# Performance work log

Measured on AMD Instinct MI355X. Metric: run time of the kernel, lower is better.

The kernel has to match this reference:

```python
import jax, jax.numpy as jnp
import numpy as np

MAX_GRAPH_SIZE = 512
HEADS = 8
DIM_HEAD = 32

N, D = 8192, 256
G, MN = 16, 512
E = 131072


def setup_inputs() -> dict:
    key = jax.random.key(0)
    ks = jax.random.split(key, 10)
    node_feature = jax.random.normal(ks[0], (N, D), jnp.float32)
    edge_feature = jax.random.normal(ks[1], (E, D), jnp.float32) * 0.1
    edge_index = jax.random.randint(ks[2], (2, E), 0, N)
    batch = (jnp.arange(N) // (N // G)).astype(jnp.int32)  # sorted graph ids, 512 nodes/graph
    dist = jax.random.randint(ks[3], (G, MN, MN), 0, MAX_GRAPH_SIZE).astype(jnp.int32)
    centrality = jax.random.normal(ks[4], (MAX_GRAPH_SIZE, D), jnp.float32) * 0.02
    dist_bias = jax.random.normal(ks[5], (MAX_GRAPH_SIZE, HEADS), jnp.float32) * 0.02
    Wq = jax.random.normal(ks[6], (D, HEADS * DIM_HEAD), jnp.float32) * 0.05
    Wkv = jax.random.normal(ks[7], (D, 2 * HEADS * DIM_HEAD), jnp.float32) * 0.05
    Wo = jax.random.normal(ks[8], (HEADS * DIM_HEAD, D), jnp.float32) * 0.05
    bo = jax.random.normal(ks[9], (D,), jnp.float32) * 0.05
    return dict(node_feature=node_feature, edge_feature=edge_feature,
                centrality=centrality, dist_bias=dist_bias,
                Wq=Wq, Wkv=Wkv, Wo=Wo, bo=bo,
                edge_index=edge_index, batch=batch, dist=dist)


def reference(node_feature, edge_feature, centrality, dist_bias, Wq, Wkv, Wo, bo,
              edge_index, batch, dist):
    n_nodes = node_feature.shape[0]
    g, mn = dist.shape[0], dist.shape[1]
    h, dh = HEADS, DIM_HEAD
    scale = dh ** -0.5

    src = edge_index[0]
    # node degree -> centrality encoding lookup (clipped to table size)
    deg = jax.ops.segment_sum(jnp.ones((src.shape[0],), jnp.int32), src,
                              num_segments=n_nodes)
    deg = jnp.minimum(deg, MAX_GRAPH_SIZE - 1)
    # scatter-add edge features onto source nodes
    edge_out = jax.ops.segment_sum(edge_feature, src, num_segments=n_nodes)
    x = node_feature + centrality[deg] + edge_out  # [N, D]

    # dense-batch pack (to_dense_batch): position of each node within its graph
    counts = jax.ops.segment_sum(jnp.ones((n_nodes,), jnp.int32), batch, num_segments=g)
    starts = jnp.cumsum(counts) - counts  # exclusive cumsum
    pos = jnp.arange(n_nodes, dtype=jnp.int32) - starts[batch]
    dense = jnp.zeros((g, mn, x.shape[1]), x.dtype).at[batch, pos].set(x)
    mask = jnp.zeros((g, mn), bool).at[batch, pos].set(True)

    # relative-distance attention bias lookup
    dist_c = jnp.minimum(dist, MAX_GRAPH_SIZE - 1)
    sim_bias = dist_bias[dist_c]  # [G, MN, MN, H]

    # multi-head attention
    q = jnp.einsum('bnd,de->bne', dense, Wq).reshape(g, mn, h, dh)
    kv = jnp.einsum('bnd,de->bne', dense, Wkv)
    k, v = jnp.split(kv, 2, axis=-1)
    k = k.reshape(g, mn, h, dh)
    v = v.reshape(g, mn, h, dh)
    sim = jnp.einsum('bihd,bjhd->bhij', q, k) * scale
    sim = sim + jnp.transpose(sim_bias, (0, 3, 1, 2))
    sim = jnp.where(mask[:, None, None, :], sim, -jnp.inf)
    attn = jax.nn.softmax(sim, axis=-1)
    out = jnp.einsum('bhij,bjhd->bihd', attn, v).reshape(g, mn, h * dh)
    pred = jnp.einsum('bne,ed->bnd', out, Wo) + bo  # [G, MN, D]

    # ragged unpack; original loop skips the last graph (off-by-one), nodes of
    # the last graph stay zero — replicated faithfully.
    new_node_features = pred[batch, pos]
    new_node_features = jnp.where((batch < g - 1)[:, None], new_node_features, 0.0)
    return new_node_features
```

## Files before the change

kernel.cpp:

```cpp
#include <hip/hip_runtime.h>
#include <hip/hip_bf16.h>
#include <math.h>

constexpr int N_   = 8192;
constexpr int D_   = 256;
constexpr int E_   = 131072;
constexpr int G_   = 16;
constexpr int MN_  = 512;
constexpr int H_   = 8;
constexpr int MAXG_= 512;

typedef __attribute__((ext_vector_type(8))) short short8v;
typedef _Float16 half8v __attribute__((ext_vector_type(8)));
typedef __attribute__((ext_vector_type(4))) float f32x4;

__device__ inline ushort f2bf(float f) {
    unsigned u = __float_as_uint(f);
    return (ushort)((u + 0x7FFFu + ((u >> 16) & 1u)) >> 16);
}
__device__ inline float bf2f(ushort h) { return __uint_as_float((unsigned)h << 16); }
__device__ inline ushort f2h(float f) {
    _Float16 h = (_Float16)f; ushort u; __builtin_memcpy(&u, &h, 2); return u;
}
__device__ inline unsigned pack_h2(float a, float b) {
    auto h = __builtin_amdgcn_cvt_pkrtz(a, b);
    unsigned u; __builtin_memcpy(&u, &h, 4); return u;
}

__global__ void k_prep0(int* __restrict__ deg, int* __restrict__ bstart) {
    int i = blockIdx.x * 256 + threadIdx.x;
    if (i < N_) deg[i] = 0;
    if (i < G_) bstart[i] = -1;
}

__device__ void wt_dev(const float* __restrict__ W, int ncols,
                       ushort* __restrict__ wth, ushort* __restrict__ wtl,
                       int bx, int by) {
    __shared__ float tile[32][33];
    int c0 = bx * 32, k0 = by * 32;
    int t = threadIdx.x;
    int tr = t >> 5, tc = t & 31;
#pragma unroll
    for (int i = 0; i < 4; ++i)
        tile[tr * 4 + i][tc] = W[(size_t)(k0 + tr * 4 + i) * ncols + c0 + tc];
    __syncthreads();
    int cr = t >> 3, kq = (t & 7) * 4;
    ushort4 hh, ll;
    float v;
    v = tile[kq + 0][cr]; hh.x = f2bf(v); ll.x = f2bf(v - bf2f(hh.x));
    v = tile[kq + 1][cr]; hh.y = f2bf(v); ll.y = f2bf(v - bf2f(hh.y));
    v = tile[kq + 2][cr]; hh.z = f2bf(v); ll.z = f2bf(v - bf2f(hh.z));
    v = tile[kq + 3][cr]; hh.w = f2bf(v); ll.w = f2bf(v - bf2f(hh.w));
    *(ushort4*)(wth + (size_t)(c0 + cr) * 256 + k0 + kq) = hh;
    *(ushort4*)(wtl + (size_t)(c0 + cr) * 256 + k0 + kq) = ll;
}

__global__ __launch_bounds__(256) void k_prep1(
    const int* __restrict__ src, int* __restrict__ deg,
    const int* __restrict__ batch, int* __restrict__ bstart,
    const float* __restrict__ Wq, const float* __restrict__ Wkv,
    const float* __restrict__ Wo,
    ushort* __restrict__ wt_h, ushort* __restrict__ wt_l,
    ushort* __restrict__ wot_h, ushort* __restrict__ wot_l) {
    int bid = blockIdx.x;
    if (bid < 512) {
        int e = bid * 256 + threadIdx.x;
        atomicAdd(deg + src[e], 1);
    } else if (bid < 544) {
        int n = (bid - 512) * 256 + threadIdx.x;
        int g = batch[n];
        if (n == 0 || batch[n - 1] != g) bstart[g] = n;
    } else {
        int wid = bid - 544;
        if (wid < 64)        wt_dev(Wq,  256, wt_h, wt_l, wid & 7, wid >> 3);
        else if (wid < 192)  wt_dev(Wkv, 512, wt_h + 256 * 256, wt_l + 256 * 256,
                                    (wid - 64) & 15, (wid - 64) >> 4);
        else                 wt_dev(Wo,  256, wot_h, wot_l, (wid - 192) & 7, (wid - 192) >> 3);
    }
}

__global__ void k_prep2(const int* __restrict__ bstart, int* __restrict__ starts,
                        int* __restrict__ counts, const int* __restrict__ deg,
                        int* __restrict__ offs, int* __restrict__ cursor) {
    int t = threadIdx.x;
    if (t == 0) {
        int next = N_;
        for (int g = G_ - 1; g >= 0; --g) {
            int b = bstart[g];
            int s = (b >= 0) ? b : next;
            starts[g] = s;
            counts[g] = next - s;
            next = s;
        }
    }
    __shared__ int sums[256];
    int base = t * 32;
    int local[32];
    int s = 0;
#pragma unroll
    for (int k = 0; k < 32; ++k) { local[k] = deg[base + k]; s += local[k]; }
    sums[t] = s;
    __syncthreads();
    for (int off = 1; off < 256; off <<= 1) {
        int v = (t >= off) ? sums[t - off] : 0;
        __syncthreads();
        sums[t] += v;
        __syncthreads();
    }
    int acc = sums[t] - s;
#pragma unroll
    for (int k = 0; k < 32; ++k) {
        offs[base + k] = acc;
        cursor[base + k] = acc;
        acc += local[k];
    }
}

__global__ void k_fill_csr(const int* __restrict__ src, int* __restrict__ cursor,
                           int* __restrict__ eids) {
    int e = blockIdx.x * 256 + threadIdx.x;
    if (e < E_) {
        int slot = atomicAdd(cursor + src[e], 1);
        eids[slot] = e;
    }
}

__global__ void k_build_dense(const float* __restrict__ nf, const float* __restrict__ cent,
                              const float* __restrict__ ef, const int* __restrict__ deg,
                              const int* __restrict__ offs, const int* __restrict__ eids,
                              const int* __restrict__ batch, const int* __restrict__ starts,
                              ushort* __restrict__ xh, ushort* __restrict__ xl) {
    int t  = blockIdx.x * 256 + threadIdx.x;
    int n  = t >> 6;
    int c4 = (t & 63) * 4;
    if (n >= N_) return;
    int g = batch[n];
    int p = n - starts[g];
    if (p >= MN_) return;
    int row = g * MN_ + p;
    int dn = deg[n];
    int dg = min(dn, MAXG_ - 1);
    float4 a = *(const float4*)(nf   + (size_t)n  * D_ + c4);
    float4 b = *(const float4*)(cent + (size_t)dg * D_ + c4);
    float4 o;
    o.x = a.x + b.x; o.y = a.y + b.y; o.z = a.z + b.z; o.w = a.w + b.w;
    int beg = offs[n], end = beg + dn;
    int idx = beg;
    for (; idx + 4 <= end; idx += 4) {
        int e0 = eids[idx], e1 = eids[idx + 1], e2 = eids[idx + 2], e3 = eids[idx + 3];
        float4 v0 = *(const float4*)(ef + (size_t)e0 * D_ + c4);
        float4 v1 = *(const float4*)(ef + (size_t)e1 * D_ + c4);
        float4 v2 = *(const float4*)(ef + (size_t)e2 * D_ + c4);
        float4 v3 = *(const float4*)(ef + (size_t)e3 * D_ + c4);
        o.x += v0.x; o.y += v0.y; o.z += v0.z; o.w += v0.w;
        o.x += v1.x; o.y += v1.y; o.z += v1.z; o.w += v1.w;
        o.x += v2.x; o.y += v2.y; o.z += v2.z; o.w += v2.w;
        o.x += v3.x; o.y += v3.y; o.z += v3.z; o.w += v3.w;
    }
    for (; idx < end; ++idx) {
        int e = eids[idx];
        float4 v = *(const float4*)(ef + (size_t)e * D_ + c4);
        o.x += v.x; o.y += v.y; o.z += v.z; o.w += v.w;
    }
    ushort4 hh, ll;
    hh.x = f2bf(o.x); ll.x = f2bf(o.x - bf2f(hh.x));
    hh.y = f2bf(o.y); ll.y = f2bf(o.y - bf2f(hh.y));
    hh.z = f2bf(o.z); ll.z = f2bf(o.z - bf2f(hh.z));
    hh.w = f2bf(o.w); ll.w = f2bf(o.w - bf2f(hh.w));
    *(ushort4*)(xh + (size_t)row * D_ + c4) = hh;
    *(ushort4*)(xl + (size_t)row * D_ + c4) = ll;
}

__global__ __launch_bounds__(256) void k_gemm_qkv(
    const ushort* __restrict__ xh, const ushort* __restrict__ xl,
    const ushort* __restrict__ wth, const ushort* __restrict__ wtl,
    ushort* __restrict__ qh, ushort* __restrict__ qlo,
    ushort* __restrict__ kh, ushort* __restrict__ klo,
    ushort* __restrict__ vt) {
    int w = threadIdx.x >> 6, lane = threadIdx.x & 63;
    int l15 = lane & 15, quad = lane >> 4;
    int m0 = blockIdx.x * 128 + w * 32;
    int nc0 = blockIdx.y * 64;
    f32x4 acc[2][4] = {};
    const ushort* a0h = xh + (size_t)(m0 + l15) * 256 + quad * 8;
    const ushort* a0l = xl + (size_t)(m0 + l15) * 256 + quad * 8;
    for (int kc = 0; kc < 256; kc += 32) {
        short8v ah0 = *(const short8v*)(a0h + kc);
        short8v al0 = *(const short8v*)(a0l + kc);
        short8v ah1 = *(const short8v*)(a0h + 16 * 256 + kc);
        short8v al1 = *(const short8v*)(a0l + 16 * 256 + kc);
#pragma unroll
        for (int c = 0; c < 4; ++c) {
            size_t bo = (size_t)(nc0 + c * 16 + l15) * 256 + kc + quad * 8;
            short8v bh = *(const short8v*)(wth + bo);
            short8v bl = *(const short8v*)(wtl + bo);
            acc[0][c] = __builtin_amdgcn_mfma_f32_16x16x32_bf16(al0, bh, acc[0][c], 0, 0, 0);
            acc[0][c] = __builtin_amdgcn_mfma_f32_16x16x32_bf16(ah0, bl, acc[0][c], 0, 0, 0);
            acc[0][c] = __builtin_amdgcn_mfma_f32_16x16x32_bf16(ah0, bh, acc[0][c], 0, 0, 0);
            acc[1][c] = __builtin_amdgcn_mfma_f32_16x16x32_bf16(al1, bh, acc[1][c], 0, 0, 0);
            acc[1][c] = __builtin_amdgcn_mfma_f32_16x16x32_bf16(ah1, bl, acc[1][c], 0, 0, 0);
            acc[1][c] = __builtin_amdgcn_mfma_f32_16x16x32_bf16(ah1, bh, acc[1][c], 0, 0, 0);
        }
    }
    int seg = nc0 >> 8;
#pragma unroll
    for (int t = 0; t < 2; ++t) {
        int m0t = m0 + t * 16;
        int g = m0t >> 9;
        int r0 = m0t + quad * 4;
#pragma unroll
        for (int c = 0; c < 4; ++c) {
            int col = nc0 + c * 16 + l15;
            if (seg == 0) {
#pragma unroll
                for (int r = 0; r < 4; ++r) {
                    float v = acc[t][c][r];
                    ushort hh = f2bf(v);
                    qh [(size_t)(r0 + r) * 256 + col] = hh;
                    qlo[(size_t)(r0 + r) * 256 + col] = f2bf(v - bf2f(hh));
                }
            } else if (seg == 1) {
                int cc = col - 256;
#pragma unroll
                for (int r = 0; r < 4; ++r) {
                    float v = acc[t][c][r];
                    ushort hh = f2bf(v);
                    kh [(size_t)(r0 + r) * 256 + cc] = hh;
                    klo[(size_t)(r0 + r) * 256 + cc] = f2bf(v - bf2f(hh));
                }
            } else {
                int cv = col - 512;
                int h = cv >> 5, d = cv & 31;
                int j0 = (m0t & 511) + quad * 4;
                ushort4 vv;
                vv.x = f2h(acc[t][c][0]); vv.y = f2h(acc[t][c][1]);
                vv.z = f2h(acc[t][c][2]); vv.w = f2h(acc[t][c][3]);
                *(ushort4*)(vt + ((size_t)((g * 8 + h) * 32 + d)) * 512 + j0) = vv;
            }
        }
    }
}

__global__ __launch_bounds__(512) void k_attn_fused(
    const ushort* __restrict__ qh, const ushort* __restrict__ qlo,
    const ushort* __restrict__ kh, const ushort* __restrict__ klo,
    const ushort* __restrict__ vt,
    const int* __restrict__ dist, const float* __restrict__ dist_bias,
    const int* __restrict__ starts, const int* __restrict__ counts,
    const ushort* __restrict__ woth, const ushort* __restrict__ wotl,
    const float* __restrict__ bo, float* __restrict__ out)
{
    __shared__ ushort dist_lds[32][272];
    __shared__ ushort olo_lds[32][264];
    __shared__ float  biasH[8][516];

    int bid = blockIdx.x;
    int b = (bid & 7) * 32 + (bid >> 3);
    int g  = b >> 4;
    int ib = (b & 15) * 32;
    int w    = threadIdx.x >> 6;
    int lane = threadIdx.x & 63;
    int l15  = lane & 15, quad = lane >> 4;
    int h = w;
    const float scale2 = 0.17677669529663687f * 1.4426950408889634f;
    const float LOG2E  = 1.4426950408889634f;

    for (int idx = threadIdx.x; idx < 4096; idx += 512)
        biasH[idx & 7][idx >> 3] = dist_bias[idx] * LOG2E;
    {
        int r = threadIdx.x >> 4;
        int c0 = (threadIdx.x & 15) * 32;
        const int* drow = dist + ((size_t)(g * 512 + ib + r)) * 512 + c0;
#pragma unroll
        for (int u = 0; u < 32; u += 8) {
            int4 da = *(const int4*)(drow + u);
            int4 db = *(const int4*)(drow + u + 4);
            ushort4 s0, s1;
            s0.x = (ushort)min(da.x, 511); s0.y = (ushort)min(da.y, 511);
            s0.z = (ushort)min(da.z, 511); s0.w = (ushort)min(da.w, 511);
            s1.x = (ushort)min(db.x, 511); s1.y = (ushort)min(db.y, 511);
            s1.z = (ushort)min(db.z, 511); s1.w = (ushort)min(db.w, 511);
            *(ushort4*)&dist_lds[r][c0 + u]     = s0;
            *(ushort4*)&dist_lds[r][c0 + u + 4] = s1;
        }
    }
    __syncthreads();
    int cnt = counts[g];

    size_t qoff = ((size_t)(g * 512 + ib + l15)) * 256 + h * 32 + quad * 8;
    short8v qfh0 = *(const short8v*)(qh  + qoff);
    short8v qfl0 = *(const short8v*)(qlo + qoff);
    short8v qfh1 = *(const short8v*)(qh  + qoff + 16 * 256);
    short8v qfl1 = *(const short8v*)(qlo + qoff + 16 * 256);

    float m0s = -INFINITY, l0s = 0.f, m1s = -INFINITY, l1s = 0.f;
    f32x4 t0a0 = {0.f,0.f,0.f,0.f}, t0a1 = {0.f,0.f,0.f,0.f};
    f32x4 t1a0 = {0.f,0.f,0.f,0.f}, t1a1 = {0.f,0.f,0.f,0.f};

    const ushort* vbase = vt + ((size_t)((g * 8 + h) * 32)) * 512;
    size_t krowb = (size_t)(g * 512);

    auto tile_step = [&](int jb, int rowoff, bool full, short8v qfh, short8v qfl,
                         float& m, float& lsum, f32x4& a0, f32x4& a1,
                         short8v kfh0, short8v kfl0, short8v kfh1, short8v kfl1,
                         half8v v0, half8v v1) {
        float p[8];
        f32x4 c0 = {0.f,0.f,0.f,0.f};
        c0 = __builtin_amdgcn_mfma_f32_16x16x32_bf16(kfl0, qfh, c0, 0, 0, 0);
        c0 = __builtin_amdgcn_mfma_f32_16x16x32_bf16(kfh0, qfl, c0, 0, 0, 0);
        c0 = __builtin_amdgcn_mfma_f32_16x16x32_bf16(kfh0, qfh, c0, 0, 0, 0);
        f32x4 c1 = {0.f,0.f,0.f,0.f};
        c1 = __builtin_amdgcn_mfma_f32_16x16x32_bf16(kfl1, qfh, c1, 0, 0, 0);
        c1 = __builtin_amdgcn_mfma_f32_16x16x32_bf16(kfh1, qfl, c1, 0, 0, 0);
        c1 = __builtin_amdgcn_mfma_f32_16x16x32_bf16(kfh1, qfh, c1, 0, 0, 0);
        ushort4 d0 = *(const ushort4*)&dist_lds[rowoff + l15][jb + quad * 4];
        ushort4 d1 = *(const ushort4*)&dist_lds[rowoff + l15][jb + 16 + quad * 4];
        const ushort* dr0 = (const ushort*)&d0;
        const ushort* dr1 = (const ushort*)&d1;
        if (full) {
#pragma unroll
            for (int r = 0; r < 4; ++r) p[r]     = c0[r] * scale2 + biasH[h][dr0[r]];
#pragma unroll
            for (int r = 0; r < 4; ++r) p[4 + r] = c1[r] * scale2 + biasH[h][dr1[r]];
        } else {
#pragma unroll
            for (int r = 0; r < 4; ++r) {
                float s = c0[r] * scale2 + biasH[h][dr0[r]];
                p[r] = ((jb + quad * 4 + r) < cnt) ? s : -1e30f;
            }
#pragma unroll
            for (int r = 0; r < 4; ++r) {
                float s = c1[r] * scale2 + biasH[h][dr1[r]];
                p[4 + r] = ((jb + 16 + quad * 4 + r) < cnt) ? s : -1e30f;
            }
        }
        float mx = fmaxf(fmaxf(fmaxf(p[0], p[1]), fmaxf(p[2], p[3])),
                         fmaxf(fmaxf(p[4], p[5]), fmaxf(p[6], p[7])));
        mx = fmaxf(mx, __shfl_xor(mx, 16));
        mx = fmaxf(mx, __shfl_xor(mx, 32));
        float mnew = fmaxf(m, mx);
        float corr = exp2f(m - mnew);
        m = mnew;
        float m10 = m - 10.f;
        if (full) {
#pragma unroll
            for (int u = 0; u < 8; ++u) p[u] = exp2f(p[u] - m10);
        } else {
#pragma unroll
            for (int u = 0; u < 8; ++u)
                p[u] = (p[u] > -1e29f) ? exp2f(p[u] - m10) : 0.f;
        }
        float psum = ((p[0] + p[1]) + (p[2] + p[3])) + ((p[4] + p[5]) + (p[6] + p[7]));
        psum += __shfl_xor(psum, 16);
        psum += __shfl_xor(psum, 32);
        lsum = lsum * corr + psum;
#pragma unroll
        for (int r = 0; r < 4; ++r) {
            float cr = __shfl(corr, quad * 4 + r);
            a0[r] *= cr; a1[r] *= cr;
        }
        unsigned pk0A = pack_h2(p[0], p[1]), pk1A = pack_h2(p[2], p[3]);
        unsigned pk0B = pack_h2(p[4], p[5]), pk1B = pack_h2(p[6], p[7]);
        int srcA = l15 + 16 * (2 * (quad & 1));
        int srcB = srcA + 16;
        unsigned w0A = __shfl((int)pk0A, srcA), w1A = __shfl((int)pk1A, srcA);
        unsigned w2A = __shfl((int)pk0A, srcB), w3A = __shfl((int)pk1A, srcB);
        unsigned w0B = __shfl((int)pk0B, srcA), w1B = __shfl((int)pk1B, srcA);
        unsigned w2B = __shfl((int)pk0B, srcB), w3B = __shfl((int)pk1B, srcB);
        bool hiT = (quad >= 2);
        union { unsigned u[4]; half8v h; } pu;
        pu.u[0] = hiT ? w0B : w0A;
        pu.u[1] = hiT ? w1B : w1A;
        pu.u[2] = hiT ? w2B : w2A;
        pu.u[3] = hiT ? w3B : w3A;
        half8v pa = pu.h;
        a0 = __builtin_amdgcn_mfma_f32_16x16x32_f16(pa, v0, a0, 0, 0, 0);
        a1 = __builtin_amdgcn_mfma_f32_16x16x32_f16(pa, v1, a1, 0, 0, 0);
    };

    for (int jb = 0; jb < 512; jb += 32) {
        bool full = (jb + 32 <= cnt);
        size_t koff = (krowb + jb + l15) * 256 + h * 32 + quad * 8;
        short8v kfh0 = *(const short8v*)(kh  + koff);
        short8v kfl0 = *(const short8v*)(klo + koff);
        short8v kfh1 = *(const short8v*)(kh  + koff + 16 * 256);
        short8v kfl1 = *(const short8v*)(klo + koff + 16 * 256);
        half8v v0 = *(const half8v*)(vbase + (size_t)l15 * 512 + jb + quad * 8);
        half8v v1 = *(const half8v*)(vbase + (size_t)(l15 + 16) * 512 + jb + quad * 8);
        tile_step(jb, 0,  full, qfh0, qfl0, m0s, l0s, t0a0, t0a1,
                  kfh0, kfl0, kfh1, kfl1, v0, v1);
        tile_step(jb, 16, full, qfh1, qfl1, m1s, l1s, t1a0, t1a1,
                  kfh0, kfl0, kfh1, kfl1, v0, v1);
    }
    float inv0 = l0s > 0.f ? 1.f / l0s : 0.f;
    float inv1 = l1s > 0.f ? 1.f / l1s : 0.f;

    __syncthreads();
    ushort* oh_lds = &dist_lds[0][0];
    ushort* ol_lds = &olo_lds[0][0];
#pragma unroll
    for (int r = 0; r < 4; ++r) {
        float ir0 = __shfl(inv0, quad * 4 + r);
        float ir1 = __shfl(inv1, quad * 4 + r);
        int i0 = quad * 4 + r;
        int i1 = 16 + quad * 4 + r;
        float o00 = t0a0[r] * ir0, o01 = t0a1[r] * ir0;
        float o10 = t1a0[r] * ir1, o11 = t1a1[r] * ir1;
        ushort h00 = f2bf(o00), h01 = f2bf(o01), h10 = f2bf(o10), h11 = f2bf(o11);
        oh_lds[i0 * 264 + h * 32 + l15]      = h00;
        ol_lds[i0 * 264 + h * 32 + l15]      = f2bf(o00 - bf2f(h00));
        oh_lds[i0 * 264 + h * 32 + 16 + l15] = h01;
        ol_lds[i0 * 264 + h * 32 + 16 + l15] = f2bf(o01 - bf2f(h01));
        oh_lds[i1 * 264 + h * 32 + l15]      = h10;
        ol_lds[i1 * 264 + h * 32 + l15]      = f2bf(o10 - bf2f(h10));
        oh_lds[i1 * 264 + h * 32 + 16 + l15] = h11;
        ol_lds[i1 * 264 + h * 32 + 16 + l15] = f2bf(o11 - bf2f(h11));
    }
    __syncthreads();

    f32x4 pacc[2][2] = {};
    for (int kc = 0; kc < 256; kc += 32) {
        short8v ah0 = *(const short8v*)(oh_lds + l15 * 264 + kc + quad * 8);
        short8v al0 = *(const short8v*)(ol_lds + l15 * 264 + kc + quad * 8);
        short8v ah1 = *(const short8v*)(oh_lds + (l15 + 16) * 264 + kc + quad * 8);
        short8v al1 = *(const short8v*)(ol_lds + (l15 + 16) * 264 + kc + quad * 8);
#pragma unroll
        for (int cc = 0; cc < 2; ++cc) {
            int col = w * 32 + cc * 16 + l15;
            size_t bof = (size_t)col * 256 + kc + quad * 8;
            short8v bh = *(const short8v*)(woth + bof);
            short8v bl = *(const short8v*)(wotl + bof);
            pacc[0][cc] = __builtin_amdgcn_mfma_f32_16x16x32_bf16(al0, bh, pacc[0][cc], 0, 0, 0);
            pacc[0][cc] = __builtin_amdgcn_mfma_f32_16x16x32_bf16(ah0, bl, pacc[0][cc], 0, 0, 0);
            pacc[0][cc] = __builtin_amdgcn_mfma_f32_16x16x32_bf16(ah0, bh, pacc[0][cc], 0, 0, 0);
            pacc[1][cc] = __builtin_amdgcn_mfma_f32_16x16x32_bf16(al1, bh, pacc[1][cc], 0, 0, 0);
            pacc[1][cc] = __builtin_amdgcn_mfma_f32_16x16x32_bf16(ah1, bl, pacc[1][cc], 0, 0, 0);
            pacc[1][cc] = __builtin_amdgcn_mfma_f32_16x16x32_bf16(ah1, bh, pacc[1][cc], 0, 0, 0);
        }
    }
    int st = starts[g];
    bool lastg = (g == G_ - 1);
#pragma unroll
    for (int rg = 0; rg < 2; ++rg) {
#pragma unroll
        for (int cc = 0; cc < 2; ++cc) {
            int col = w * 32 + cc * 16 + l15;
            float bias = bo[col];
#pragma unroll
            for (int r = 0; r < 4; ++r) {
                int prow = ib + rg * 16 + quad * 4 + r;
                if (prow < cnt)
                    out[(size_t)(st + prow) * 256 + col] = lastg ? 0.f : (pacc[rg][cc][r] + bias);
            }
        }
    }
}

extern "C" void kernel_launch(void* const* d_in, const int* in_sizes, int n_in,
                              void* d_out, int out_size, void* d_ws, size_t ws_size,
                              hipStream_t stream) {
    const float* node_feature = (const float*)d_in[0];
    const float* edge_feature = (const float*)d_in[1];
    const float* centrality   = (const float*)d_in[2];
    const float* dist_bias    = (const float*)d_in[3];
    const float* Wq           = (const float*)d_in[4];
    const float* Wkv          = (const float*)d_in[5];
    const float* Wo           = (const float*)d_in[6];
    const float* bo           = (const float*)d_in[7];
    const int*   edge_index   = (const int*)d_in[8];
    const int*   batch        = (const int*)d_in[9];
    const int*   dist         = (const int*)d_in[10];
    float* out = (float*)d_out;

    const size_t ND = (size_t)N_ * D_;
    ushort* xh   = (ushort*)d_ws;
    ushort* xl   = xh  + ND;
    ushort* qh   = xl  + ND;
    ushort* qlo  = qh  + ND;
    ushort* kh   = qlo + ND;
    ushort* klo  = kh  + ND;
    ushort* vt   = klo + ND;
    ushort* wt_h = vt  + ND;
    ushort* wt_l = wt_h + (size_t)768 * 256;
    ushort* wot_h= wt_l + (size_t)768 * 256;
    ushort* wot_l= wot_h + (size_t)256 * 256;
    int* deg    = (int*)(wot_l + (size_t)256 * 256);
    int* bstart = deg + N_;
    int* counts = bstart + G_;
    int* starts = counts + G_;
    int* offs   = starts + G_;
    int* cursor = offs + N_;
    int* eids   = cursor + N_;

    const int* src = edge_index;

    k_prep0<<<N_ / 256, 256, 0, stream>>>(deg, bstart);
    k_prep1<<<800, 256, 0, stream>>>(src, deg, batch, bstart, Wq, Wkv, Wo,
                                     wt_h, wt_l, wot_h, wot_l);
    k_prep2<<<1, 256, 0, stream>>>(bstart, starts, counts, deg, offs, cursor);
    k_fill_csr<<<E_ / 256, 256, 0, stream>>>(src, cursor, eids);
    k_build_dense<<<(N_ * 64) / 256, 256, 0, stream>>>(node_feature, centrality, edge_feature,
                                                       deg, offs, eids, batch, starts, xh, xl);
    k_gemm_qkv<<<dim3(64, 12), 256, 0, stream>>>(xh, xl, wt_h, wt_l,
                                                 qh, qlo, kh, klo, vt);
    k_attn_fused<<<256, 512, 0, stream>>>(qh, qlo, kh, klo, vt, dist, dist_bias,
                                          starts, counts, wot_h, wot_l, bo, out);
}
```

Before: 139.6 us.

## Split fused attention into per-head split-K attention plus separate output projection GEMM

The fused attention kernel, which processed all 8 heads of a 32-row block in one 512-thread workgroup and did the output projection in LDS, is replaced. Attention now runs with one workgroup per (graph, head, 64-row block), and the key range is split between wave pairs whose softmax partial states are merged through LDS. This gives 1024 smaller workgroups for better occupancy. A separate pre-pass converts dist to clipped 16-bit values, and a standalone GEMM applies Wo and the bias. The cost is an extra global round trip for the attention output, two added kernel launches, and dist being read per head from global or L2 rather than staged once in LDS.

```diff
diff --git a/kernel.cpp b/kernel.cpp
--- a/kernel.cpp
+++ b/kernel.cpp
@@ -123,6 +123,19 @@
         int slot = atomicAdd(cursor + src[e], 1);
         eids[slot] = e;
     }
+}
+
+__global__ void k_dist16(const int* __restrict__ dist, ushort* __restrict__ dbuf) {
+    size_t i = ((size_t)blockIdx.x * 256 + threadIdx.x) * 8;
+    int4 a = *(const int4*)(dist + i);
+    int4 b = *(const int4*)(dist + i + 4);
+    ushort4 s0, s1;
+    s0.x = (ushort)min(a.x, 511); s0.y = (ushort)min(a.y, 511);
+    s0.z = (ushort)min(a.z, 511); s0.w = (ushort)min(a.w, 511);
+    s1.x = (ushort)min(b.x, 511); s1.y = (ushort)min(b.y, 511);
+    s1.z = (ushort)min(b.z, 511); s1.w = (ushort)min(b.w, 511);
+    *(ushort4*)(dbuf + i)     = s0;
+    *(ushort4*)(dbuf + i + 4) = s1;
 }
 
 __global__ void k_build_dense(const float* __restrict__ nf, const float* __restrict__ cent,
@@ -241,53 +254,37 @@
     }
 }
 
-__global__ __launch_bounds__(512) void k_attn_fused(
+__global__ __launch_bounds__(256) void k_attn2(
     const ushort* __restrict__ qh, const ushort* __restrict__ qlo,
     const ushort* __restrict__ kh, const ushort* __restrict__ klo,
-    const ushort* __restrict__ vt,
-    const int* __restrict__ dist, const float* __restrict__ dist_bias,
-    const int* __restrict__ starts, const int* __restrict__ counts,
-    const ushort* __restrict__ woth, const ushort* __restrict__ wotl,
-    const float* __restrict__ bo, float* __restrict__ out)
+    const ushort* __restrict__ vt, const ushort* __restrict__ dbuf,
+    const float* __restrict__ dist_bias, const int* __restrict__ counts,
+    ushort* __restrict__ oh_g, ushort* __restrict__ ol_g)
 {
-    __shared__ ushort dist_lds[32][272];
-    __shared__ ushort olo_lds[32][264];
-    __shared__ float  biasH[8][516];
+    __shared__ float bias_lds[512];
+    __shared__ float ml_lds[2][2][16][2];
+    __shared__ float acc_lds[2][64][16];
 
     int bid = blockIdx.x;
-    int b = (bid & 7) * 32 + (bid >> 3);
-    int g  = b >> 4;
-    int ib = (b & 15) * 32;
-    int w    = threadIdx.x >> 6;
+    int b = (bid & 7) * 128 + (bid >> 3);
+    int g   = b >> 6;
+    int rem = b & 63;
+    int h   = rem >> 3;
+    int iq  = rem & 7;
+    int wv   = threadIdx.x >> 6;
     int lane = threadIdx.x & 63;
-    int l15  = lane & 15, quad = lane >> 4;
-    int h = w;
+    int it = wv & 1, jh = wv >> 1;
+    int l15 = lane & 15, quad = lane >> 4;
+    int ibw = iq * 64 + it * 32;
     const float scale2 = 0.17677669529663687f * 1.4426950408889634f;
     const float LOG2E  = 1.4426950408889634f;
 
-    for (int idx = threadIdx.x; idx < 4096; idx += 512)
-        biasH[idx & 7][idx >> 3] = dist_bias[idx] * LOG2E;
-    {
-        int r = threadIdx.x >> 4;
-        int c0 = (threadIdx.x & 15) * 32;
-        const int* drow = dist + ((size_t)(g * 512 + ib + r)) * 512 + c0;
-#pragma unroll
-        for (int u = 0; u < 32; u += 8) {
-            int4 da = *(const int4*)(drow + u);
-            int4 db = *(const int4*)(drow + u + 4);
-            ushort4 s0, s1;
-            s0.x = (ushort)min(da.x, 511); s0.y = (ushort)min(da.y, 511);
-            s0.z = (ushort)min(da.z, 511); s0.w = (ushort)min(da.w, 511);
-            s1.x = (ushort)min(db.x, 511); s1.y = (ushort)min(db.y, 511);
-            s1.z = (ushort)min(db.z, 511); s1.w = (ushort)min(db.w, 511);
-            *(ushort4*)&dist_lds[r][c0 + u]     = s0;
-            *(ushort4*)&dist_lds[r][c0 + u + 4] = s1;
-        }
-    }
+    for (int idx = threadIdx.x; idx < 512; idx += 256)
+        bias_lds[idx] = dist_bias[idx * 8 + h] * LOG2E;
     __syncthreads();
     int cnt = counts[g];
 
-    size_t qoff = ((size_t)(g * 512 + ib + l15)) * 256 + h * 32 + quad * 8;
+    size_t qoff = ((size_t)(g * 512 + ibw + l15)) * 256 + h * 32 + quad * 8;
     short8v qfh0 = *(const short8v*)(qh  + qoff);
     short8v qfl0 = *(const short8v*)(qlo + qoff);
     short8v qfh1 = *(const short8v*)(qh  + qoff + 16 * 256);
@@ -298,9 +295,12 @@
     f32x4 t1a0 = {0.f,0.f,0.f,0.f}, t1a1 = {0.f,0.f,0.f,0.f};
 
     const ushort* vbase = vt + ((size_t)((g * 8 + h) * 32)) * 512;
+    const ushort* dR0 = dbuf + ((size_t)(g * 512 + ibw + l15)) * 512;
+    const ushort* dR1 = dR0 + (size_t)16 * 512;
     size_t krowb = (size_t)(g * 512);
 
-    auto tile_step = [&](int jb, int rowoff, bool full, short8v qfh, short8v qfl,
+    auto tile_step = [&](int jb, const ushort* dRow, bool full,
+                         short8v qfh, short8v qfl,
                          float& m, float& lsum, f32x4& a0, f32x4& a1,
                          short8v kfh0, short8v kfl0, short8v kfh1, short8v kfl1,
                          half8v v0, half8v v1) {
@@ -313,24 +313,24 @@
         c1 = __builtin_amdgcn_mfma_f32_16x16x32_bf16(kfl1, qfh, c1, 0, 0, 0);
         c1 = __builtin_amdgcn_mfma_f32_16x16x32_bf16(kfh1, qfl, c1, 0, 0, 0);
         c1 = __builtin_amdgcn_mfma_f32_16x16x32_bf16(kfh1, qfh, c1, 0, 0, 0);
-        ushort4 d0 = *(const ushort4*)&dist_lds[rowoff + l15][jb + quad * 4];
-        ushort4 d1 = *(const ushort4*)&dist_lds[rowoff + l15][jb + 16 + quad * 4];
+        ushort4 d0 = *(const ushort4*)(dRow + jb + quad * 4);
+        ushort4 d1 = *(const ushort4*)(dRow + jb + 16 + quad * 4);
         const ushort* dr0 = (const ushort*)&d0;
         const ushort* dr1 = (const ushort*)&d1;
         if (full) {
 #pragma unroll
-            for (int r = 0; r < 4; ++r) p[r]     = c0[r] * scale2 + biasH[h][dr0[r]];
-#pragma unroll
-            for (int r = 0; r < 4; ++r) p[4 + r] = c1[r] * scale2 + biasH[h][dr1[r]];
+            for (int r = 0; r < 4; ++r) p[r]     = c0[r] * scale2 + bias_lds[dr0[r]];
+#pragma unroll
+            for (int r = 0; r < 4; ++r) p[4 + r] = c1[r] * scale2 + bias_lds[dr1[r]];
         } else {
 #pragma unroll
             for (int r = 0; r < 4; ++r) {
-                float s = c0[r] * scale2 + biasH[h][dr0[r]];
+                float s = c0[r] * scale2 + bias_lds[dr0[r]];
                 p[r] = ((jb + quad * 4 + r) < cnt) ? s : -1e30f;
             }
 #pragma unroll
             for (int r = 0; r < 4; ++r) {
-                float s = c1[r] * scale2 + biasH[h][dr1[r]];
+                float s = c1[r] * scale2 + bias_lds[dr1[r]];
                 p[4 + r] = ((jb + 16 + quad * 4 + r) < cnt) ? s : -1e30f;
             }
         }
@@ -368,17 +368,18 @@
         unsigned w0B = __shfl((int)pk0B, srcA), w1B = __shfl((int)pk1B, srcA);
         unsigned w2B = __shfl((int)pk0B, srcB), w3B = __shfl((int)pk1B, srcB);
         bool hiT = (quad >= 2);
-        union { unsigned u[4]; half8v h; } pu;
+        union { unsigned u[4]; half8v hh; } pu;
         pu.u[0] = hiT ? w0B : w0A;
         pu.u[1] = hiT ? w1B : w1A;
         pu.u[2] = hiT ? w2B : w2A;
         pu.u[3] = hiT ? w3B : w3A;
-        half8v pa = pu.h;
+        half8v pa = pu.hh;
         a0 = __builtin_amdgcn_mfma_f32_16x16x32_f16(pa, v0, a0, 0, 0, 0);
         a1 = __builtin_amdgcn_mfma_f32_16x16x32_f16(pa, v1, a1, 0, 0, 0);
     };
 
-    for (int jb = 0; jb < 512; jb += 32) {
+    int jlo = jh * 256, jhi = jlo + 256;
+    for (int jb = jlo; jb < jhi; jb += 32) {
         bool full = (jb + 32 <= cnt);
         size_t koff = (krowb + jb + l15) * 256 + h * 32 + quad * 8;
         short8v kfh0 = *(const short8v*)(kh  + koff);
@@ -387,71 +388,96 @@
         short8v kfl1 = *(const short8v*)(klo + koff + 16 * 256);
         half8v v0 = *(const half8v*)(vbase + (size_t)l15 * 512 + jb + quad * 8);
         half8v v1 = *(const half8v*)(vbase + (size_t)(l15 + 16) * 512 + jb + quad * 8);
-        tile_step(jb, 0,  full, qfh0, qfl0, m0s, l0s, t0a0, t0a1,
+        tile_step(jb, dR0, full, qfh0, qfl0, m0s, l0s, t0a0, t0a1,
                   kfh0, kfl0, kfh1, kfl1, v0, v1);
-        tile_step(jb, 16, full, qfh1, qfl1, m1s, l1s, t1a0, t1a1,
+        tile_step(jb, dR1, full, qfh1, qfl1, m1s, l1s, t1a0, t1a1,
                   kfh0, kfl0, kfh1, kfl1, v0, v1);
     }
-    float inv0 = l0s > 0.f ? 1.f / l0s : 0.f;
-    float inv1 = l1s > 0.f ? 1.f / l1s : 0.f;
-
+
+    if (jh == 1) {
+        if (quad == 0) {
+            ml_lds[it][0][l15][0] = m0s; ml_lds[it][0][l15][1] = l0s;
+            ml_lds[it][1][l15][0] = m1s; ml_lds[it][1][l15][1] = l1s;
+        }
+        float* ap = &acc_lds[it][lane][0];
+#pragma unroll
+        for (int r = 0; r < 4; ++r) {
+            ap[r]      = t0a0[r];
+            ap[4 + r]  = t0a1[r];
+            ap[8 + r]  = t1a0[r];
+            ap[12 + r] = t1a1[r];
+        }
+    }
     __syncthreads();
-    ushort* oh_lds = &dist_lds[0][0];
-    ushort* ol_lds = &olo_lds[0][0];
-#pragma unroll
-    for (int r = 0; r < 4; ++r) {
-        float ir0 = __shfl(inv0, quad * 4 + r);
-        float ir1 = __shfl(inv1, quad * 4 + r);
-        int i0 = quad * 4 + r;
-        int i1 = 16 + quad * 4 + r;
-        float o00 = t0a0[r] * ir0, o01 = t0a1[r] * ir0;
-        float o10 = t1a0[r] * ir1, o11 = t1a1[r] * ir1;
-        ushort h00 = f2bf(o00), h01 = f2bf(o01), h10 = f2bf(o10), h11 = f2bf(o11);
-        oh_lds[i0 * 264 + h * 32 + l15]      = h00;
-        ol_lds[i0 * 264 + h * 32 + l15]      = f2bf(o00 - bf2f(h00));
-        oh_lds[i0 * 264 + h * 32 + 16 + l15] = h01;
-        ol_lds[i0 * 264 + h * 32 + 16 + l15] = f2bf(o01 - bf2f(h01));
-        oh_lds[i1 * 264 + h * 32 + l15]      = h10;
-        ol_lds[i1 * 264 + h * 32 + l15]      = f2bf(o10 - bf2f(h10));
-        oh_lds[i1 * 264 + h * 32 + 16 + l15] = h11;
-        ol_lds[i1 * 264 + h * 32 + 16 + l15] = f2bf(o11 - bf2f(h11));
-    }
-    __syncthreads();
-
-    f32x4 pacc[2][2] = {};
+    if (jh == 0) {
+        float mp0 = ml_lds[it][0][l15][0], lp0 = ml_lds[it][0][l15][1];
+        float mp1 = ml_lds[it][1][l15][0], lp1 = ml_lds[it][1][l15][1];
+        float mt0 = fmaxf(m0s, mp0), mt1 = fmaxf(m1s, mp1);
+        float ss0 = exp2f(m0s - mt0), sp0 = exp2f(mp0 - mt0);
+        float ss1 = exp2f(m1s - mt1), sp1 = exp2f(mp1 - mt1);
+        float lt0 = l0s * ss0 + lp0 * sp0;
+        float lt1 = l1s * ss1 + lp1 * sp1;
+        float inv0 = lt0 > 0.f ? 1.f / lt0 : 0.f;
+        float inv1 = lt1 > 0.f ? 1.f / lt1 : 0.f;
+        const float* ap = &acc_lds[it][lane][0];
+#pragma unroll
+        for (int r = 0; r < 4; ++r) {
+            int q4r = quad * 4 + r;
+            float a0s = __shfl(ss0, q4r), a0p = __shfl(sp0, q4r), ir0 = __shfl(inv0, q4r);
+            float a1s = __shfl(ss1, q4r), a1p = __shfl(sp1, q4r), ir1 = __shfl(inv1, q4r);
+            float o00 = (t0a0[r] * a0s + ap[r]      * a0p) * ir0;
+            float o01 = (t0a1[r] * a0s + ap[4 + r]  * a0p) * ir0;
+            float o10 = (t1a0[r] * a1s + ap[8 + r]  * a1p) * ir1;
+            float o11 = (t1a1[r] * a1s + ap[12 + r] * a1p) * ir1;
+            size_t row0 = (size_t)(g * 512 + ibw + quad * 4 + r) * 256 + h * 32;
+            size_t row1 = row0 + (size_t)16 * 256;
+            ushort h00 = f2bf(o00), h01 = f2bf(o01), h10 = f2bf(o10), h11 = f2bf(o11);
+            oh_g[row0 + l15]      = h00; ol_g[row0 + l15]      = f2bf(o00 - bf2f(h00));
+            oh_g[row0 + 16 + l15] = h01; ol_g[row0 + 16 + l15] = f2bf(o01 - bf2f(h01));
+            oh_g[row1 + l15]      = h10; ol_g[row1 + l15]      = f2bf(o10 - bf2f(h10));
+            oh_g[row1 + 16 + l15] = h11; ol_g[row1 + 16 + l15] = f2bf(o11 - bf2f(h11));
+        }
+    }
+}
+
+__global__ __launch_bounds__(256) void k_gemm_proj(
+    const ushort* __restrict__ oh, const ushort* __restrict__ ol,
+    const ushort* __restrict__ woth, const ushort* __restrict__ wotl,
+    const float* __restrict__ bo, const int* __restrict__ starts,
+    const int* __restrict__ counts, float* __restrict__ out) {
+    int w = threadIdx.x >> 6, lane = threadIdx.x & 63;
+    int l15 = lane & 15, quad = lane >> 4;
+    int m0 = blockIdx.x * 64 + w * 16;
+    int nc0 = blockIdx.y * 64;
+    f32x4 acc[4] = {};
+    const ushort* ah_p = oh + (size_t)(m0 + l15) * 256 + quad * 8;
+    const ushort* al_p = ol + (size_t)(m0 + l15) * 256 + quad * 8;
     for (int kc = 0; kc < 256; kc += 32) {
-        short8v ah0 = *(const short8v*)(oh_lds + l15 * 264 + kc + quad * 8);
-        short8v al0 = *(const short8v*)(ol_lds + l15 * 264 + kc + quad * 8);
-        short8v ah1 = *(const short8v*)(oh_lds + (l15 + 16) * 264 + kc + quad * 8);
-        short8v al1 = *(const short8v*)(ol_lds + (l15 + 16) * 264 + kc + quad * 8);
-#pragma unroll
-        for (int cc = 0; cc < 2; ++cc) {
-            int col = w * 32 + cc * 16 + l15;
-            size_t bof = (size_t)col * 256 + kc + quad * 8;
+        short8v ah = *(const short8v*)(ah_p + kc);
+        short8v al = *(const short8v*)(al_p + kc);
+#pragma unroll
+        for (int c = 0; c < 4; ++c) {
+            size_t bof = (size_t)(nc0 + c * 16 + l15) * 256 + kc + quad * 8;
             short8v bh = *(const short8v*)(woth + bof);
             short8v bl = *(const short8v*)(wotl + bof);
-            pacc[0][cc] = __builtin_amdgcn_mfma_f32_16x16x32_bf16(al0, bh, pacc[0][cc], 0, 0, 0);
-            pacc[0][cc] = __builtin_amdgcn_mfma_f32_16x16x32_bf16(ah0, bl, pacc[0][cc], 0, 0, 0);
-            pacc[0][cc] = __builtin_amdgcn_mfma_f32_16x16x32_bf16(ah0, bh, pacc[0][cc], 0, 0, 0);
-            pacc[1][cc] = __builtin_amdgcn_mfma_f32_16x16x32_bf16(al1, bh, pacc[1][cc], 0, 0, 0);
-            pacc[1][cc] = __builtin_amdgcn_mfma_f32_16x16x32_bf16(ah1, bl, pacc[1][cc], 0, 0, 0);
-            pacc[1][cc] = __builtin_amdgcn_mfma_f32_16x16x32_bf16(ah1, bh, pacc[1][cc], 0, 0, 0);
-        }
-    }
-    int st = starts[g];
+            acc[c] = __builtin_amdgcn_mfma_f32_16x16x32_bf16(al, bh, acc[c], 0, 0, 0);
+            acc[c] = __builtin_amdgcn_mfma_f32_16x16x32_bf16(ah, bl, acc[c], 0, 0, 0);
+            acc[c] = __builtin_amdgcn_mfma_f32_16x16x32_bf16(ah, bh, acc[c], 0, 0, 0);
+        }
+    }
+    int g = m0 >> 9;
+    int cnt = counts[g], st = starts[g];
     bool lastg = (g == G_ - 1);
-#pragma unroll
-    for (int rg = 0; rg < 2; ++rg) {
-#pragma unroll
-        for (int cc = 0; cc < 2; ++cc) {
-            int col = w * 32 + cc * 16 + l15;
-            float bias = bo[col];
-#pragma unroll
-            for (int r = 0; r < 4; ++r) {
-                int prow = ib + rg * 16 + quad * 4 + r;
-                if (prow < cnt)
-                    out[(size_t)(st + prow) * 256 + col] = lastg ? 0.f : (pacc[rg][cc][r] + bias);
-            }
+    int p0 = (m0 & 511) + quad * 4;
+#pragma unroll
+    for (int c = 0; c < 4; ++c) {
+        int col = nc0 + c * 16 + l15;
+        float bias = bo[col];
+#pragma unroll
+        for (int r = 0; r < 4; ++r) {
+            int p = p0 + r;
+            if (p < cnt)
+                out[(size_t)(st + p) * 256 + col] = lastg ? 0.f : (acc[c][r] + bias);
         }
     }
 }
@@ -480,7 +506,10 @@
     ushort* kh   = qlo + ND;
     ushort* klo  = kh  + ND;
     ushort* vt   = klo + ND;
-    ushort* wt_h = vt  + ND;
+    ushort* dbuf = vt  + ND;
+    ushort* oh_g = dbuf + (size_t)G_ * MN_ * MN_;
+    ushort* ol_g = oh_g + ND;
+    ushort* wt_h = ol_g + ND;
     ushort* wt_l = wt_h + (size_t)768 * 256;
     ushort* wot_h= wt_l + (size_t)768 * 256;
     ushort* wot_l= wot_h + (size_t)256 * 256;
@@ -499,10 +528,13 @@
                                      wt_h, wt_l, wot_h, wot_l);
     k_prep2<<<1, 256, 0, stream>>>(bstart, starts, counts, deg, offs, cursor);
     k_fill_csr<<<E_ / 256, 256, 0, stream>>>(src, cursor, eids);
+    k_dist16<<<(G_ * MN_ * MN_) / (256 * 8), 256, 0, stream>>>(dist, dbuf);
     k_build_dense<<<(N_ * 64) / 256, 256, 0, stream>>>(node_feature, centrality, edge_feature,
                                                        deg, offs, eids, batch, starts, xh, xl);
     k_gemm_qkv<<<dim3(64, 12), 256, 0, stream>>>(xh, xl, wt_h, wt_l,
                                                  qh, qlo, kh, klo, vt);
-    k_attn_fused<<<256, 512, 0, stream>>>(qh, qlo, kh, klo, vt, dist, dist_bias,
-                                          starts, counts, wot_h, wot_l, bo, out);
-}
+    k_attn2<<<1024, 256, 0, stream>>>(qh, qlo, kh, klo, vt, dbuf, dist_bias,
+                                      counts, oh_g, ol_g);
+    k_gemm_proj<<<dim3(128, 4), 256, 0, stream>>>(oh_g, ol_g, wot_h, wot_l,
+                                                  bo, starts, counts, out);
+}
```

Result: slower. 168.8 us (+21.0%).
